# Optimization experiments

Measured on AMD Instinct MI355X. Metric: run time of the kernel, lower is better.

## Reference

```python
import jax, jax.numpy as jnp
import numpy as np

TEMPERATURE = 0.5

def setup_inputs() -> dict:
    key = jax.random.key(0)
    k1, k2 = jax.random.split(key)
    B, D = 4096, 512
    z_anchor = jax.random.normal(k1, (B, D), dtype=jnp.float32)
    z_positive = jax.random.normal(k2, (B, D), dtype=jnp.float32)
    return {"z_anchor": z_anchor, "z_positive": z_positive}

def reference(z_anchor, z_positive):
    B = z_anchor.shape[0]
    N = 2 * B
    z = jnp.concatenate([z_anchor, z_positive], axis=0)            # [2B, D]
    # Cosine similarity via normalize-once + GEMM (same math as broadcasted
    # F.cosine_similarity with eps=1e-8 clamp on norms).
    norms = jnp.maximum(jnp.linalg.norm(z, axis=1, keepdims=True), 1e-8)
    zn = z / norms                                                  # [2B, D]
    cos = zn @ zn.T                                                 # [2B, 2B]
    logits = cos / TEMPERATURE
    # mask self-similarity on the diagonal with -inf
    diag = jnp.eye(N, dtype=bool)
    logits = jnp.where(diag, -jnp.inf, logits)
    labels = jnp.concatenate([jnp.arange(B, N), jnp.arange(B)])     # positive index per row
    # cross-entropy: mean(logsumexp(row) - row[label])
    lse = jax.nn.logsumexp(logits, axis=1)                          # [2B]
    pos_logit = jnp.take_along_axis(logits, labels[:, None], axis=1)[:, 0]
    loss = jnp.mean(lse - pos_logit)
    # ---- metrics (no-grad diagnostics) ----
    predictions = jnp.argmax(logits, axis=1)
    accuracy = jnp.mean((predictions == labels).astype(jnp.float32))
    zan = z_anchor / jnp.maximum(jnp.linalg.norm(z_anchor, axis=1, keepdims=True), 1e-8)
    zpn = z_positive / jnp.maximum(jnp.linalg.norm(z_positive, axis=1, keepdims=True), 1e-8)
    pos_sim = jnp.mean(jnp.sum(zan * zpn, axis=1))
    # off-diagonal mean of cosine sims (diag entries are exactly 1 after normalize)
    neg_sim = (jnp.sum(cos) - jnp.trace(cos)) / (N * (N - 1))
    z_std = jnp.mean(jnp.std(z, axis=0, ddof=1))                    # torch unbiased std
    z_mean_norm = jnp.linalg.norm(jnp.mean(z, axis=0))
    return (loss, accuracy, pos_sim, neg_sim, z_std, z_mean_norm)
```

## Files before the change

### kernel.cpp

```cpp
#include <hip/hip_runtime.h>
#include <stdint.h>

#define NROWS 8192
#define BHALF 4096
#define DIM 512
#define NBLK 64
#define NTRI 2080
#define NRIDER 64
#define ZWORDS 26112

typedef __attribute__((ext_vector_type(8))) _Float16 f16x8;
typedef __attribute__((ext_vector_type(4))) float f32x4;

__device__ __forceinline__ void gload_lds16(const void* g, void* l) {
  __builtin_amdgcn_global_load_lds(
      (const __attribute__((address_space(1))) unsigned int*)g,
      (__attribute__((address_space(3))) unsigned int*)l, 16, 0, 0);
}

extern "C" __global__ __launch_bounds__(256) void k_prep(
    const float* __restrict__ za, const float* __restrict__ zp,
    unsigned short* __restrict__ zf,
    float* __restrict__ inv_norms, float* __restrict__ partials,
    uint32_t* __restrict__ zbase32)
{
  {
    int idx = blockIdx.x * 26 + threadIdx.x;
    if (threadIdx.x < 26 && idx < ZWORDS) zbase32[idx] = 0u;
  }
  __shared__ float tr_sh[4], pd_sh[4];
  const int wid = threadIdx.x >> 6, lane = threadIdx.x & 63;
  const int i = blockIdx.x * 4 + wid;
  const float4* a4 = (const float4*)(za + (size_t)i * DIM);
  const float4* p4 = (const float4*)(zp + (size_t)i * DIM);
  float4 a0 = a4[lane * 2], a1 = a4[lane * 2 + 1];
  float4 p0 = p4[lane * 2], p1 = p4[lane * 2 + 1];
  float xa[8] = {a0.x, a0.y, a0.z, a0.w, a1.x, a1.y, a1.z, a1.w};
  float xp[8] = {p0.x, p0.y, p0.z, p0.w, p1.x, p1.y, p1.z, p1.w};
  float ssa = 0.f, ssp = 0.f;
#pragma unroll
  for (int j = 0; j < 8; ++j) { ssa += xa[j] * xa[j]; ssp += xp[j] * xp[j]; }
#pragma unroll
  for (int m = 1; m < 64; m <<= 1) {
    ssa += __shfl_xor(ssa, m, 64);
    ssp += __shfl_xor(ssp, m, 64);
  }
  float na = fmaxf(sqrtf(ssa), 1e-8f), np_ = fmaxf(sqrtf(ssp), 1e-8f);
  float ia = 1.0f / na, ip = 1.0f / np_;
  float pd = 0.f;
  unsigned short ua[8], up[8];
#pragma unroll
  for (int j = 0; j < 8; ++j) {
    float zna = xa[j] * ia, znp = xp[j] * ip;
    pd += zna * znp;
    _Float16 hza = (_Float16)zna, hzp = (_Float16)znp;
    ua[j] = __builtin_bit_cast(unsigned short, hza);
    up[j] = __builtin_bit_cast(unsigned short, hzp);
  }
#pragma unroll
  for (int m = 1; m < 64; m <<= 1) pd += __shfl_xor(pd, m, 64);
  float tr = ssa * ia * ia + ssp * ip * ip;
  if (lane == 0) {
    tr_sh[wid] = tr; pd_sh[wid] = pd;
    inv_norms[i] = ia; inv_norms[i + BHALF] = ip;
  }
  uint4 va = {(uint32_t)ua[0] | ((uint32_t)ua[1] << 16), (uint32_t)ua[2] | ((uint32_t)ua[3] << 16),
              (uint32_t)ua[4] | ((uint32_t)ua[5] << 16), (uint32_t)ua[6] | ((uint32_t)ua[7] << 16)};
  uint4 vp = {(uint32_t)up[0] | ((uint32_t)up[1] << 16), (uint32_t)up[2] | ((uint32_t)up[3] << 16),
              (uint32_t)up[4] | ((uint32_t)up[5] << 16), (uint32_t)up[6] | ((uint32_t)up[7] << 16)};
  ((uint4*)(zf + (size_t)i * DIM))[lane] = va;
  ((uint4*)(zf + (size_t)(i + BHALF) * DIM))[lane] = vp;
  __syncthreads();
  if (threadIdx.x == 0) {
    partials[blockIdx.x * 2]     = tr_sh[0] + tr_sh[1] + tr_sh[2] + tr_sh[3];
    partials[blockIdx.x * 2 + 1] = pd_sh[0] + pd_sh[1] + pd_sh[2] + pd_sh[3];
  }
}

extern "C" __global__ __launch_bounds__(256) void k_gemm(
    const unsigned short* __restrict__ zf,
    const float* __restrict__ za, const float* __restrict__ zp,
    const float* __restrict__ inv_norms,
    float* __restrict__ sumexp, unsigned long long* __restrict__ amax,
    float* __restrict__ colsum, float* __restrict__ colsumsq,
    float* __restrict__ snorm)
{
  __shared__ char lds[32768] __attribute__((aligned(128)));

  if (blockIdx.x < NRIDER) {
    const int c = threadIdx.x;
    const int r0 = blockIdx.x * 128;
    const float* src = (r0 < BHALF) ? (za + (size_t)r0 * DIM)
                                    : (zp + (size_t)(r0 - BHALF) * DIM);
    float s0 = 0.f, q0 = 0.f, n0 = 0.f, s1 = 0.f, q1 = 0.f, n1 = 0.f;
#pragma unroll 4
    for (int rr = 0; rr < 128; ++rr) {
      float v0 = src[(size_t)rr * DIM + c];
      float v1 = src[(size_t)rr * DIM + c + 256];
      float inv = inv_norms[r0 + rr];
      s0 += v0; q0 += v0 * v0; n0 += v0 * inv;
      s1 += v1; q1 += v1 * v1; n1 += v1 * inv;
    }
    atomicAdd(&colsum[c], s0);      atomicAdd(&colsum[c + 256], s1);
    atomicAdd(&colsumsq[c], q0);    atomicAdd(&colsumsq[c + 256], q1);
    atomicAdd(&snorm[c], n0);       atomicAdd(&snorm[c + 256], n1);
    return;
  }

  const int tid = threadIdx.x;
  const int wid = tid >> 6, lane = tid & 63;
  const int wr = wid >> 1, wc = wid & 1;
  const int fr = lane & 15, s0l = lane >> 4, fq = lane >> 4;

  const int raw = blockIdx.x - NRIDER;
  const int t = (raw & 7) * 260 + (raw >> 3);
  int bj = (int)((sqrtf(8.0f * (float)t + 1.0f) - 1.0f) * 0.5f);
  while (bj < NBLK - 1 && (bj + 1) * (bj + 2) / 2 <= t) ++bj;
  while (bj > 0 && bj * (bj + 1) / 2 > t) --bj;
  const int bi = t - bj * (bj + 1) / 2;
  const int rowA = bi * 128, rowB = bj * 128;

  uint32_t goff[8];
#pragma unroll
  for (int s = 0; s < 8; ++s) {
    int c = wid * 8 + s;
    int p = c >> 4;
    int off = (c & 15) * 1024 + lane * 16;
    int r = off >> 7;
    int sl = ((off >> 4) & 7) ^ (r & 7);
    int Lb = (sl << 4) | (off & 15);
    uint32_t grow = (uint32_t)((p ? rowB : rowA) + r);
    goff[s] = grow * (uint32_t)DIM + (uint32_t)(Lb >> 1);
  }

  const int x = fr & 7;
  const int slk0 = ((s0l) ^ x) << 4;
  const int slk1 = ((4 + s0l) ^ x) << 4;
  const int abase = (wr * 64 + fr) * 128;
  const int bbase = 16384 + (wc * 64 + fr) * 128;

  f32x4 acc[4][4];
#pragma unroll
  for (int m = 0; m < 4; ++m)
#pragma unroll
    for (int n = 0; n < 4; ++n) acc[m][n] = (f32x4){0.f, 0.f, 0.f, 0.f};

  for (int kt = 0; kt < 8; ++kt) {
    if (kt) __syncthreads();
#pragma unroll
    for (int s = 0; s < 8; ++s) {
      int c = wid * 8 + s;
      gload_lds16(zf + goff[s] + kt * 64,
                  (char*)lds + (c >> 4) * 16384 + (c & 15) * 1024);
    }
    __syncthreads();

#pragma unroll
    for (int ks = 0; ks < 2; ++ks) {
      const int slk = ks ? slk1 : slk0;
      f16x8 a[4], b[4];
#pragma unroll
      for (int m = 0; m < 4; ++m)
        a[m] = *(const f16x8*)((const char*)lds + abase + m * 2048 + slk);
#pragma unroll
      for (int n = 0; n < 4; ++n)
        b[n] = *(const f16x8*)((const char*)lds + bbase + n * 2048 + slk);
#pragma unroll
      for (int m = 0; m < 4; ++m)
#pragma unroll
        for (int n = 0; n < 4; ++n)
          acc[m][n] = __builtin_amdgcn_mfma_f32_16x16x32_f16(a[m], b[n], acc[m][n], 0, 0, 0);
    }
  }

#pragma unroll
  for (int m = 0; m < 4; ++m) {
#pragma unroll
    for (int rr = 0; rr < 4; ++rr) {
      int gi = rowA + wr * 64 + m * 16 + fq * 4 + rr;
      float se = 0.f;
      unsigned long long best = 0ull;
#pragma unroll
      for (int n = 0; n < 4; ++n) {
        int gj = rowB + wc * 64 + n * 16 + fr;
        if (gi != gj) {
          float logit = 2.0f * acc[m][n][rr];
          se += __expf(logit);
          uint32_t bu = __float_as_uint(logit);
          uint32_t sk = (bu & 0x80000000u) ? ~bu : (bu | 0x80000000u);
          unsigned long long pk =
              ((unsigned long long)sk << 32) | (uint32_t)(~(uint32_t)gj);
          if (pk > best) best = pk;
        }
      }
#pragma unroll
      for (int msk = 1; msk < 16; msk <<= 1) {
        se += __shfl_xor(se, msk, 64);
        unsigned long long o = __shfl_xor(best, msk, 64);
        if (o > best) best = o;
      }
      if (fr == 0) {
        atomicAdd(&sumexp[gi], se);
        atomicMax(&amax[gi], best);
      }
    }
  }

  if (bi != bj) {
#pragma unroll
    for (int n = 0; n < 4; ++n) {
      int gj = rowB + wc * 64 + n * 16 + fr;
      float se = 0.f;
      unsigned long long best = 0ull;
#pragma unroll
      for (int m = 0; m < 4; ++m) {
#pragma unroll
        for (int rr = 0; rr < 4; ++rr) {
          int gi = rowA + wr * 64 + m * 16 + fq * 4 + rr;
          float logit = 2.0f * acc[m][n][rr];
          se += __expf(logit);
          uint32_t bu = __float_as_uint(logit);
          uint32_t sk = (bu & 0x80000000u) ? ~bu : (bu | 0x80000000u);
          unsigned long long pk =
              ((unsigned long long)sk << 32) | (uint32_t)(~(uint32_t)gi);
          if (pk > best) best = pk;
        }
      }
#pragma unroll
      for (int msk = 16; msk < 64; msk <<= 1) {
        se += __shfl_xor(se, msk, 64);
        unsigned long long o = __shfl_xor(best, msk, 64);
        if (o > best) best = o;
      }
      if (fq == 0) {
        atomicAdd(&sumexp[gj], se);
        atomicMax(&amax[gj], best);
      }
    }
  }
}

extern "C" __global__ __launch_bounds__(1024) void k_final(
    const float* __restrict__ sumexp, const unsigned long long* __restrict__ amax,
    const float* __restrict__ colsum, const float* __restrict__ colsumsq,
    const float* __restrict__ snorm, const float* __restrict__ partials,
    float* __restrict__ out)
{
  __shared__ double red[1024];
  const int t = threadIdx.x;
  double lsesum = 0.0, cnt = 0.0;
  for (int r = t; r < NROWS; r += 1024) {
    lsesum += log((double)sumexp[r]);
    int label = (r < BHALF) ? r + BHALF : r - BHALF;
    unsigned int idx = ~(unsigned int)(amax[r] & 0xffffffffull);
    if ((int)idx == label) cnt += 1.0;
  }
  double stdsum = 0, mn2 = 0, sn2 = 0;
  for (int c = t; c < DIM; c += 1024) {
    double su = colsum[c], sq = colsumsq[c];
    double var = (sq - su * su / 8192.0) / 8191.0;
    stdsum += sqrt(var > 0.0 ? var : 0.0);
    double m = su / 8192.0; mn2 += m * m;
    double s = snorm[c];   sn2 += s * s;
  }
  double trp = 0.0, pdp = 0.0;
  if (t < 1024) {
    trp = partials[t * 2];
    pdp = partials[t * 2 + 1];
  }
  auto red_sum = [&](double v) -> double {
    __syncthreads();
    red[t] = v; __syncthreads();
    for (int s = 512; s > 0; s >>= 1) {
      if (t < s) red[t] += red[t + s];
      __syncthreads();
    }
    return red[0];
  };
  double Tlse = red_sum(lsesum);
  double Tcnt = red_sum(cnt);
  double Tstd = red_sum(stdsum);
  double Tmn2 = red_sum(mn2);
  double Tsn2 = red_sum(sn2);
  double Ttr  = red_sum(trp);
  double Tpd  = red_sum(pdp);
  if (t == 0) {
    double pos_sim = Tpd / 4096.0;
    out[0] = (float)(Tlse / 8192.0 - 2.0 * pos_sim);
    out[1] = (float)(Tcnt / 8192.0);
    out[2] = (float)pos_sim;
    out[3] = (float)((Tsn2 - Ttr) / (8192.0 * 8191.0));
    out[4] = (float)(Tstd / 512.0);
    out[5] = (float)sqrt(Tmn2);
  }
}

extern "C" void kernel_launch(void* const* d_in, const int* in_sizes, int n_in,
                              void* d_out, int out_size, void* d_ws, size_t ws_size,
                              hipStream_t stream) {
  const float* za = (const float*)d_in[0];
  const float* zp = (const float*)d_in[1];
  float* out = (float*)d_out;
  char* ws = (char*)d_ws;
  size_t off = 0;
  unsigned short* zf = (unsigned short*)(ws + off); off += (size_t)NROWS * DIM * 2;
  float* inv_norms = (float*)(ws + off); off += (size_t)NROWS * 4;
  char* zbase = ws + off;
  float* sumexp = (float*)(ws + off); off += (size_t)NROWS * 4;
  unsigned long long* amax = (unsigned long long*)(ws + off); off += (size_t)NROWS * 8;
  float* colsum = (float*)(ws + off); off += (size_t)DIM * 4;
  float* colsumsq = (float*)(ws + off); off += (size_t)DIM * 4;
  float* snorm = (float*)(ws + off); off += (size_t)DIM * 4;
  float* partials = (float*)(ws + off); off += 2048 * 4;

  k_prep<<<dim3(1024), dim3(256), 0, stream>>>(za, zp, zf, inv_norms,
                                               partials, (uint32_t*)zbase);
  k_gemm<<<dim3(NTRI + NRIDER), dim3(256), 0, stream>>>(
      zf, za, zp, inv_norms, sumexp, amax, colsum, colsumsq, snorm);
  k_final<<<dim3(1), dim3(1024), 0, stream>>>(sumexp, amax, colsum, colsumsq,
                                              snorm, partials, out);
}
```

Measured before the change: 151.2 us.

## Double-buffer GEMM LDS loads and fuse final reduction via last-block counter

Doubles the LDS tile buffer so the next K-slice is prefetched with global_load_lds while MFMAs consume the current one, with one barrier per iteration and raised wave priority around the MFMA block. The separate k_final launch is removed; the last block to finish, found through an atomic done counter, performs the final reduction with 256 threads. The epilogue is rewritten to compute row and column partial sums and argmax in a single pass, using float/index shuffles instead of 64-bit packed keys. The larger LDS footprint can lower occupancy, and the done counter must be zeroed by the existing workspace init, which is extended by 16 words.

After: 305.2 us. +101.9%, slower.

```diff
diff --git a/kernel.cpp b/kernel.cpp
--- a/kernel.cpp
+++ b/kernel.cpp
@@ -1,5 +1,6 @@
 #include <hip/hip_runtime.h>
 #include <stdint.h>
+#include <math.h>
 
 #define NROWS 8192
 #define BHALF 4096
@@ -7,7 +8,8 @@
 #define NBLK 64
 #define NTRI 2080
 #define NRIDER 64
-#define ZWORDS 26112
+#define NTOT (NTRI + NRIDER)
+#define ZWORDS 26128
 
 typedef __attribute__((ext_vector_type(8))) _Float16 f16x8;
 typedef __attribute__((ext_vector_type(4))) float f32x4;
@@ -83,9 +85,11 @@
     const float* __restrict__ inv_norms,
     float* __restrict__ sumexp, unsigned long long* __restrict__ amax,
     float* __restrict__ colsum, float* __restrict__ colsumsq,
-    float* __restrict__ snorm)
+    float* __restrict__ snorm, const float* __restrict__ partials,
+    uint32_t* __restrict__ done, float* __restrict__ out)
 {
-  __shared__ char lds[32768] __attribute__((aligned(128)));
+  __shared__ char lds[2 * 32768] __attribute__((aligned(128)));
+  __shared__ uint32_t rank_sh;
 
   if (blockIdx.x < NRIDER) {
     const int c = threadIdx.x;
@@ -104,194 +108,221 @@
     atomicAdd(&colsum[c], s0);      atomicAdd(&colsum[c + 256], s1);
     atomicAdd(&colsumsq[c], q0);    atomicAdd(&colsumsq[c + 256], q1);
     atomicAdd(&snorm[c], n0);       atomicAdd(&snorm[c + 256], n1);
-    return;
-  }
-
-  const int tid = threadIdx.x;
-  const int wid = tid >> 6, lane = tid & 63;
-  const int wr = wid >> 1, wc = wid & 1;
-  const int fr = lane & 15, s0l = lane >> 4, fq = lane >> 4;
-
-  const int raw = blockIdx.x - NRIDER;
-  const int t = (raw & 7) * 260 + (raw >> 3);
-  int bj = (int)((sqrtf(8.0f * (float)t + 1.0f) - 1.0f) * 0.5f);
-  while (bj < NBLK - 1 && (bj + 1) * (bj + 2) / 2 <= t) ++bj;
-  while (bj > 0 && bj * (bj + 1) / 2 > t) --bj;
-  const int bi = t - bj * (bj + 1) / 2;
-  const int rowA = bi * 128, rowB = bj * 128;
-
-  uint32_t goff[8];
-#pragma unroll
-  for (int s = 0; s < 8; ++s) {
-    int c = wid * 8 + s;
-    int p = c >> 4;
-    int off = (c & 15) * 1024 + lane * 16;
-    int r = off >> 7;
-    int sl = ((off >> 4) & 7) ^ (r & 7);
-    int Lb = (sl << 4) | (off & 15);
-    uint32_t grow = (uint32_t)((p ? rowB : rowA) + r);
-    goff[s] = grow * (uint32_t)DIM + (uint32_t)(Lb >> 1);
-  }
-
-  const int x = fr & 7;
-  const int slk0 = ((s0l) ^ x) << 4;
-  const int slk1 = ((4 + s0l) ^ x) << 4;
-  const int abase = (wr * 64 + fr) * 128;
-  const int bbase = 16384 + (wc * 64 + fr) * 128;
-
-  f32x4 acc[4][4];
-#pragma unroll
-  for (int m = 0; m < 4; ++m)
-#pragma unroll
-    for (int n = 0; n < 4; ++n) acc[m][n] = (f32x4){0.f, 0.f, 0.f, 0.f};
-
-  for (int kt = 0; kt < 8; ++kt) {
-    if (kt) __syncthreads();
+  } else {
+    const int tid = threadIdx.x;
+    const int wid = tid >> 6, lane = tid & 63;
+    const int wr = wid >> 1, wc = wid & 1;
+    const int fr = lane & 15, s0l = lane >> 4, fq = lane >> 4;
+
+    const int raw = blockIdx.x - NRIDER;
+    const int t = (raw & 7) * 260 + (raw >> 3);
+    int bj = (int)((sqrtf(8.0f * (float)t + 1.0f) - 1.0f) * 0.5f);
+    while (bj < NBLK - 1 && (bj + 1) * (bj + 2) / 2 <= t) ++bj;
+    while (bj > 0 && bj * (bj + 1) / 2 > t) --bj;
+    const int bi = t - bj * (bj + 1) / 2;
+    const int rowA = bi * 128, rowB = bj * 128;
+
+    uint32_t goff[8];
 #pragma unroll
     for (int s = 0; s < 8; ++s) {
       int c = wid * 8 + s;
-      gload_lds16(zf + goff[s] + kt * 64,
-                  (char*)lds + (c >> 4) * 16384 + (c & 15) * 1024);
-    }
-    __syncthreads();
-
-#pragma unroll
-    for (int ks = 0; ks < 2; ++ks) {
-      const int slk = ks ? slk1 : slk0;
-      f16x8 a[4], b[4];
+      int p = c >> 4;
+      int off = (c & 15) * 1024 + lane * 16;
+      int r = off >> 7;
+      int sl = ((off >> 4) & 7) ^ (r & 7);
+      int Lb = (sl << 4) | (off & 15);
+      uint32_t grow = (uint32_t)((p ? rowB : rowA) + r);
+      goff[s] = grow * (uint32_t)DIM + (uint32_t)(Lb >> 1);
+    }
+
+    const int x = fr & 7;
+    const int slk0 = ((s0l) ^ x) << 4;
+    const int slk1 = ((4 + s0l) ^ x) << 4;
+    const int abase = (wr * 64 + fr) * 128;
+    const int bbase = 16384 + (wc * 64 + fr) * 128;
+
+    f32x4 acc[4][4];
+#pragma unroll
+    for (int m = 0; m < 4; ++m)
+#pragma unroll
+      for (int n = 0; n < 4; ++n) acc[m][n] = (f32x4){0.f, 0.f, 0.f, 0.f};
+
+#define STAGE(BUF, KT) do {                                                \
+    char* D_ = (char*)lds + (BUF) * 32768;                                 \
+    _Pragma("unroll") for (int s_ = 0; s_ < 8; ++s_) {                     \
+      int c_ = wid * 8 + s_;                                               \
+      gload_lds16(zf + goff[s_] + (KT) * 64,                               \
+                  D_ + (c_ >> 4) * 16384 + (c_ & 15) * 1024);              \
+    }                                                                      \
+  } while (0)
+
+    STAGE(0, 0);
+
+#pragma unroll 2
+    for (int kt = 0; kt < 8; ++kt) {
+      const int buf = kt & 1;
+      asm volatile("s_waitcnt lgkmcnt(0)" ::: "memory");
+      asm volatile("s_waitcnt vmcnt(0)" ::: "memory");
+      __builtin_amdgcn_sched_barrier(0);
+      __builtin_amdgcn_s_barrier();
+      __builtin_amdgcn_sched_barrier(0);
+      if (kt < 7) STAGE(buf ^ 1, kt + 1);
+      const char* Lb = (const char*)lds + buf * 32768;
+      f16x8 a0[4], b0[4], a1[4], b1[4];
+#pragma unroll
+      for (int m = 0; m < 4; ++m) {
+        a0[m] = *(const f16x8*)(Lb + abase + m * 2048 + slk0);
+        a1[m] = *(const f16x8*)(Lb + abase + m * 2048 + slk1);
+      }
+#pragma unroll
+      for (int n = 0; n < 4; ++n) {
+        b0[n] = *(const f16x8*)(Lb + bbase + n * 2048 + slk0);
+        b1[n] = *(const f16x8*)(Lb + bbase + n * 2048 + slk1);
+      }
+      __builtin_amdgcn_s_setprio(1);
 #pragma unroll
       for (int m = 0; m < 4; ++m)
-        a[m] = *(const f16x8*)((const char*)lds + abase + m * 2048 + slk);
-#pragma unroll
-      for (int n = 0; n < 4; ++n)
-        b[n] = *(const f16x8*)((const char*)lds + bbase + n * 2048 + slk);
+#pragma unroll
+        for (int n = 0; n < 4; ++n)
+          acc[m][n] = __builtin_amdgcn_mfma_f32_16x16x32_f16(a0[m], b0[n], acc[m][n], 0, 0, 0);
 #pragma unroll
       for (int m = 0; m < 4; ++m)
 #pragma unroll
         for (int n = 0; n < 4; ++n)
-          acc[m][n] = __builtin_amdgcn_mfma_f32_16x16x32_f16(a[m], b[n], acc[m][n], 0, 0, 0);
-    }
-  }
-
-#pragma unroll
-  for (int m = 0; m < 4; ++m) {
-#pragma unroll
-    for (int rr = 0; rr < 4; ++rr) {
-      int gi = rowA + wr * 64 + m * 16 + fq * 4 + rr;
-      float se = 0.f;
-      unsigned long long best = 0ull;
+          acc[m][n] = __builtin_amdgcn_mfma_f32_16x16x32_f16(a1[m], b1[n], acc[m][n], 0, 0, 0);
+      __builtin_amdgcn_s_setprio(0);
+    }
+#undef STAGE
+
+    const bool isdiag = (bi == bj);
+    float rse[4][4], rv[4][4]; int ri[4][4];
+    float cse[4], cv[4]; int ci[4];
+#pragma unroll
+    for (int n = 0; n < 4; ++n) { cse[n] = 0.f; cv[n] = -INFINITY; ci[n] = 0; }
+#pragma unroll
+    for (int m = 0; m < 4; ++m)
+#pragma unroll
+      for (int rr = 0; rr < 4; ++rr) { rse[m][rr] = 0.f; rv[m][rr] = -INFINITY; ri[m][rr] = 0; }
+
+#pragma unroll
+    for (int m = 0; m < 4; ++m) {
+#pragma unroll
+      for (int rr = 0; rr < 4; ++rr) {
+        const int gi = rowA + wr * 64 + m * 16 + fq * 4 + rr;
+#pragma unroll
+        for (int n = 0; n < 4; ++n) {
+          const int gj = rowB + wc * 64 + n * 16 + fr;
+          float lg = 2.0f * acc[m][n][rr];
+          if (isdiag && gi == gj) lg = -INFINITY;
+          float e = __expf(lg);
+          rse[m][rr] += e;
+          cse[n] += e;
+          if (lg > rv[m][rr]) { rv[m][rr] = lg; ri[m][rr] = gj; }
+          if (lg > cv[n])     { cv[n] = lg;     ci[n] = gi; }
+        }
+      }
+    }
+
+#pragma unroll
+    for (int m = 0; m < 4; ++m) {
+#pragma unroll
+      for (int rr = 0; rr < 4; ++rr) {
+        float se = rse[m][rr], v = rv[m][rr]; int idx = ri[m][rr];
+#pragma unroll
+        for (int msk = 1; msk < 16; msk <<= 1) {
+          float ose = __shfl_xor(se, msk, 64);
+          float ov  = __shfl_xor(v, msk, 64);
+          int   oi  = __shfl_xor(idx, msk, 64);
+          se += ose;
+          if (ov > v || (ov == v && oi < idx)) { v = ov; idx = oi; }
+        }
+        if (fr == 0) {
+          const int gi = rowA + wr * 64 + m * 16 + fq * 4 + rr;
+          uint32_t bu = __float_as_uint(v);
+          uint32_t key = bu ^ ((uint32_t)((int32_t)bu >> 31) | 0x80000000u);
+          unsigned long long pk = ((unsigned long long)key << 32) | (uint32_t)(~(uint32_t)idx);
+          atomicAdd(&sumexp[gi], se);
+          atomicMax(&amax[gi], pk);
+        }
+      }
+    }
+
+    if (!isdiag) {
 #pragma unroll
       for (int n = 0; n < 4; ++n) {
-        int gj = rowB + wc * 64 + n * 16 + fr;
-        if (gi != gj) {
-          float logit = 2.0f * acc[m][n][rr];
-          se += __expf(logit);
-          uint32_t bu = __float_as_uint(logit);
-          uint32_t sk = (bu & 0x80000000u) ? ~bu : (bu | 0x80000000u);
-          unsigned long long pk =
-              ((unsigned long long)sk << 32) | (uint32_t)(~(uint32_t)gj);
-          if (pk > best) best = pk;
-        }
-      }
-#pragma unroll
-      for (int msk = 1; msk < 16; msk <<= 1) {
-        se += __shfl_xor(se, msk, 64);
-        unsigned long long o = __shfl_xor(best, msk, 64);
-        if (o > best) best = o;
-      }
-      if (fr == 0) {
-        atomicAdd(&sumexp[gi], se);
-        atomicMax(&amax[gi], best);
-      }
-    }
-  }
-
-  if (bi != bj) {
-#pragma unroll
-    for (int n = 0; n < 4; ++n) {
-      int gj = rowB + wc * 64 + n * 16 + fr;
-      float se = 0.f;
-      unsigned long long best = 0ull;
-#pragma unroll
-      for (int m = 0; m < 4; ++m) {
-#pragma unroll
-        for (int rr = 0; rr < 4; ++rr) {
-          int gi = rowA + wr * 64 + m * 16 + fq * 4 + rr;
-          float logit = 2.0f * acc[m][n][rr];
-          se += __expf(logit);
-          uint32_t bu = __float_as_uint(logit);
-          uint32_t sk = (bu & 0x80000000u) ? ~bu : (bu | 0x80000000u);
-          unsigned long long pk =
-              ((unsigned long long)sk << 32) | (uint32_t)(~(uint32_t)gi);
-          if (pk > best) best = pk;
-        }
-      }
-#pragma unroll
-      for (int msk = 16; msk < 64; msk <<= 1) {
-        se += __shfl_xor(se, msk, 64);
-        unsigned long long o = __shfl_xor(best, msk, 64);
-        if (o > best) best = o;
-      }
-      if (fq == 0) {
-        atomicAdd(&sumexp[gj], se);
-        atomicMax(&amax[gj], best);
-      }
-    }
-  }
-}
-
-extern "C" __global__ __launch_bounds__(1024) void k_final(
-    const float* __restrict__ sumexp, const unsigned long long* __restrict__ amax,
-    const float* __restrict__ colsum, const float* __restrict__ colsumsq,
-    const float* __restrict__ snorm, const float* __restrict__ partials,
-    float* __restrict__ out)
-{
-  __shared__ double red[1024];
-  const int t = threadIdx.x;
-  double lsesum = 0.0, cnt = 0.0;
-  for (int r = t; r < NROWS; r += 1024) {
-    lsesum += log((double)sumexp[r]);
-    int label = (r < BHALF) ? r + BHALF : r - BHALF;
-    unsigned int idx = ~(unsigned int)(amax[r] & 0xffffffffull);
-    if ((int)idx == label) cnt += 1.0;
-  }
-  double stdsum = 0, mn2 = 0, sn2 = 0;
-  for (int c = t; c < DIM; c += 1024) {
-    double su = colsum[c], sq = colsumsq[c];
-    double var = (sq - su * su / 8192.0) / 8191.0;
-    stdsum += sqrt(var > 0.0 ? var : 0.0);
-    double m = su / 8192.0; mn2 += m * m;
-    double s = snorm[c];   sn2 += s * s;
-  }
-  double trp = 0.0, pdp = 0.0;
-  if (t < 1024) {
-    trp = partials[t * 2];
-    pdp = partials[t * 2 + 1];
-  }
-  auto red_sum = [&](double v) -> double {
-    __syncthreads();
-    red[t] = v; __syncthreads();
-    for (int s = 512; s > 0; s >>= 1) {
-      if (t < s) red[t] += red[t + s];
+        float se = cse[n], v = cv[n]; int idx = ci[n];
+#pragma unroll
+        for (int msk = 16; msk < 64; msk <<= 1) {
+          float ose = __shfl_xor(se, msk, 64);
+          float ov  = __shfl_xor(v, msk, 64);
+          int   oi  = __shfl_xor(idx, msk, 64);
+          se += ose;
+          if (ov > v || (ov == v && oi < idx)) { v = ov; idx = oi; }
+        }
+        if (fq == 0) {
+          const int gj = rowB + wc * 64 + n * 16 + fr;
+          uint32_t bu = __float_as_uint(v);
+          uint32_t key = bu ^ ((uint32_t)((int32_t)bu >> 31) | 0x80000000u);
+          unsigned long long pk = ((unsigned long long)key << 32) | (uint32_t)(~(uint32_t)idx);
+          atomicAdd(&sumexp[gj], se);
+          atomicMax(&amax[gj], pk);
+        }
+      }
+    }
+  }
+
+  __threadfence();
+  if (threadIdx.x == 0) rank_sh = atomicAdd(done, 1u);
+  __syncthreads();
+  if (rank_sh == NTOT - 1) {
+    __threadfence();
+    double* red = (double*)lds;
+    const int t = threadIdx.x;
+    double lsesum = 0.0, cnt = 0.0;
+    for (int r = t; r < NROWS; r += 256) {
+      lsesum += log((double)sumexp[r]);
+      int label = (r < BHALF) ? r + BHALF : r - BHALF;
+      unsigned int idx = ~(unsigned int)(amax[r] & 0xffffffffull);
+      if ((int)idx == label) cnt += 1.0;
+    }
+    double stdsum = 0, mn2 = 0, sn2 = 0;
+    for (int c = t; c < DIM; c += 256) {
+      double su = colsum[c], sq = colsumsq[c];
+      double var = (sq - su * su / 8192.0) / 8191.0;
+      stdsum += sqrt(var > 0.0 ? var : 0.0);
+      double m = su / 8192.0; mn2 += m * m;
+      double s = snorm[c];   sn2 += s * s;
+    }
+    double trp = 0.0, pdp = 0.0;
+    for (int b = t; b < 1024; b += 256) {
+      trp += partials[b * 2];
+      pdp += partials[b * 2 + 1];
+    }
+    auto red_sum = [&](double v) -> double {
       __syncthreads();
-    }
-    return red[0];
-  };
-  double Tlse = red_sum(lsesum);
-  double Tcnt = red_sum(cnt);
-  double Tstd = red_sum(stdsum);
-  double Tmn2 = red_sum(mn2);
-  double Tsn2 = red_sum(sn2);
-  double Ttr  = red_sum(trp);
-  double Tpd  = red_sum(pdp);
-  if (t == 0) {
-    double pos_sim = Tpd / 4096.0;
-    out[0] = (float)(Tlse / 8192.0 - 2.0 * pos_sim);
-    out[1] = (float)(Tcnt / 8192.0);
-    out[2] = (float)pos_sim;
-    out[3] = (float)((Tsn2 - Ttr) / (8192.0 * 8191.0));
-    out[4] = (float)(Tstd / 512.0);
-    out[5] = (float)sqrt(Tmn2);
+      red[t] = v; __syncthreads();
+      for (int s = 128; s > 0; s >>= 1) {
+        if (t < s) red[t] += red[t + s];
+        __syncthreads();
+      }
+      return red[0];
+    };
+    double Tlse = red_sum(lsesum);
+    double Tcnt = red_sum(cnt);
+    double Tstd = red_sum(stdsum);
+    double Tmn2 = red_sum(mn2);
+    double Tsn2 = red_sum(sn2);
+    double Ttr  = red_sum(trp);
+    double Tpd  = red_sum(pdp);
+    if (t == 0) {
+      double pos_sim = Tpd / 4096.0;
+      out[0] = (float)(Tlse / 8192.0 - 2.0 * pos_sim);
+      out[1] = (float)(Tcnt / 8192.0);
+      out[2] = (float)pos_sim;
+      out[3] = (float)((Tsn2 - Ttr) / (8192.0 * 8191.0));
+      out[4] = (float)(Tstd / 512.0);
+      out[5] = (float)sqrt(Tmn2);
+    }
   }
 }
 
@@ -311,12 +342,12 @@
   float* colsum = (float*)(ws + off); off += (size_t)DIM * 4;
   float* colsumsq = (float*)(ws + off); off += (size_t)DIM * 4;
   float* snorm = (float*)(ws + off); off += (size_t)DIM * 4;
+  uint32_t* done = (uint32_t*)(ws + off); off += 64;
   float* partials = (float*)(ws + off); off += 2048 * 4;
 
   k_prep<<<dim3(1024), dim3(256), 0, stream>>>(za, zp, zf, inv_norms,
                                                partials, (uint32_t*)zbase);
-  k_gemm<<<dim3(NTRI + NRIDER), dim3(256), 0, stream>>>(
-      zf, za, zp, inv_norms, sumexp, amax, colsum, colsumsq, snorm);
-  k_final<<<dim3(1), dim3(1024), 0, stream>>>(sumexp, amax, colsum, colsumsq,
-                                              snorm, partials, out);
+  k_gemm<<<dim3(NTOT), dim3(256), 0, stream>>>(
+      zf, za, zp, inv_norms, sumexp, amax, colsum, colsumsq, snorm,
+      partials, done, out);
 }
```
